# Performance work log

Hardware: AMD Instinct MI355X
Metric: run time of the kernel (lower is better)

## Reference

```python
import jax, jax.numpy as jnp
import numpy as np
import math

B, N, T, CI, CO = 4, 2048, 64, 32, 32
K, TAU = 6, 3


def _cheb(x, gso, k_order):
    # x: [b,n,t,c] complex, gso: [n,n] complex -> [K,b,n,t,c]
    polys = [x]
    if k_order > 1:
        polys.append(jnp.einsum('nm,bmtc->bntc', gso, x))
    for _ in range(2, k_order):
        polys.append(2.0 * jnp.einsum('nm,bmtc->bntc', gso, polys[-1]) - polys[-2])
    return jnp.stack(polys)


def _lag(p, tau):
    # shift along time axis (-2) by tau, zero-padding at the front
    if tau == 0:
        return p
    pad = jnp.zeros_like(p[..., :tau, :])
    return jnp.concatenate([pad, p[..., :-tau, :]], axis=-2)


def setup_inputs() -> dict:
    key = jax.random.key(0)
    ks = jax.random.split(key, 6)
    scale = 1.0 / math.sqrt(K * TAU * CI)
    gso_scale = 0.5 / math.sqrt(N)  # keep spectral radius ~<=1 for Cheb recursion
    return {
        'x_real': jax.random.normal(ks[0], (B, N, T, CI), jnp.float32),
        'x_imag': jax.random.normal(ks[1], (B, N, T, CI), jnp.float32),
        'gso_real': jax.random.normal(ks[2], (N, N), jnp.float32) * gso_scale,
        'gso_imag': jax.random.normal(ks[3], (N, N), jnp.float32) * gso_scale,
        'weight_real': jax.random.uniform(ks[4], (K, TAU, CI, CO), jnp.float32, -scale, scale),
        'weight_imag': jax.random.uniform(ks[5], (K, TAU, CI, CO), jnp.float32, -scale, scale),
        'bias_real': jnp.zeros((CO,), jnp.float32),
        'bias_imag': jnp.zeros((CO,), jnp.float32),
    }


def reference(x_real, x_imag, gso_real, gso_imag, weight_real, weight_imag, bias_real, bias_imag):
    x = jax.lax.complex(x_real, x_imag)
    gso = jax.lax.complex(gso_real, gso_imag)
    w = jax.lax.complex(weight_real, weight_imag)  # [K,TAU,i,o]
    bias = jax.lax.complex(bias_real, bias_imag)
    # Lag (time shift) and the graph shift act on different axes, so they
    # commute: compute the Chebyshev recursion ONCE on x, then lag the
    # stacked polynomials — same math as cheb(lag(x)) in the original.
    polys = _cheb(x, gso, K)  # [K,b,n,t,c]
    out = jnp.zeros((B, N, T, CO), dtype=polys.dtype)
    for tau in range(TAU):
        out = out + jnp.einsum('kbnti,kio->bnto', _lag(polys, tau), w[:, tau])
    return out + bias
```

## Files before the change

kernel.cpp:

```cpp
#include <hip/hip_runtime.h>
#include <stdint.h>

#define Bn 4
#define Nn 2048
#define Tn 64
#define CIn 32
#define COn 32
#define Kn 6
#define TAUn 3
#define Jn 8192

typedef _Float16 f16;
typedef _Float16 f16x2 __attribute__((ext_vector_type(2)));
typedef _Float16 f16x4 __attribute__((ext_vector_type(4)));
typedef _Float16 f16x8 __attribute__((ext_vector_type(8)));
typedef float f32x4 __attribute__((ext_vector_type(4)));

#if defined(__has_builtin)
#if __has_builtin(__builtin_amdgcn_fdot2)
#define HAVE_FDOT2 1
#endif
#endif

__device__ __forceinline__ float fdot2(f16x2 a, f16x2 b, float c) {
#ifdef HAVE_FDOT2
  return __builtin_amdgcn_fdot2(a, b, c, false);
#else
  return c + (float)a[0] * (float)b[0] + (float)a[1] * (float)b[1];
#endif
}

__device__ __forceinline__ void gld_lds16(const void* g, void* l) {
  auto gp = (const __attribute__((address_space(1))) uint32_t*)(uintptr_t)g;
  auto lp = (__attribute__((address_space(3))) uint32_t*)(uint32_t)(uintptr_t)l;
  __builtin_amdgcn_global_load_lds(gp, lp, 16, 0, 0);
}

__global__ __launch_bounds__(256) void pack_gso(const float* __restrict__ gr,
                                                const float* __restrict__ gi,
                                                f16* __restrict__ Gr,
                                                f16* __restrict__ Gi) {
  int u = blockIdx.x * 256 + threadIdx.x;
  float4 vr = ((const float4*)gr)[u];
  float4 vi = ((const float4*)gi)[u];
  f16x4 hr, hi;
  hr[0] = (f16)vr.x; hr[1] = (f16)vr.y; hr[2] = (f16)vr.z; hr[3] = (f16)vr.w;
  hi[0] = (f16)vi.x; hi[1] = (f16)vi.y; hi[2] = (f16)vi.z; hi[3] = (f16)vi.w;
  ((f16x4*)Gr)[u] = hr;
  ((f16x4*)Gi)[u] = hi;
}

__global__ __launch_bounds__(256) void pack_x(const float* __restrict__ xr,
                                              const float* __restrict__ xi,
                                              f16* __restrict__ P0) {
  __shared__ float tile[64][65];
  const int t = threadIdx.x;
  const int q0 = blockIdx.x * 64;
  const int n0 = blockIdx.y * 64;
  const int b = blockIdx.z;
  const int rr = t >> 4;
  const int cc = (t & 15) * 4;
  #pragma unroll
  for (int plane = 0; plane < 2; ++plane) {
    const float* src = plane ? xi : xr;
    if (plane) __syncthreads();
    #pragma unroll
    for (int it = 0; it < 4; ++it) {
      int n = it * 16 + rr;
      float4 v = *(const float4*)(src + ((size_t)b * Nn + n0 + n) * 2048 + q0 + cc);
      tile[n][cc + 0] = v.x; tile[n][cc + 1] = v.y;
      tile[n][cc + 2] = v.z; tile[n][cc + 3] = v.w;
    }
    __syncthreads();
    #pragma unroll
    for (int it = 0; it < 4; ++it) {
      int q = it * 16 + rr;
      f16x4 hv;
      hv[0] = (f16)tile[cc + 0][q];
      hv[1] = (f16)tile[cc + 1][q];
      hv[2] = (f16)tile[cc + 2][q];
      hv[3] = (f16)tile[cc + 3][q];
      *(f16x4*)(P0 + ((size_t)b * 2048 + q0 + q) * 4096 + plane * 2048 + n0 + cc) = hv;
    }
  }
}

__global__ __launch_bounds__(256) void pack_w(const float* __restrict__ wr,
                                              const float* __restrict__ wi,
                                              uint2* __restrict__ wpk) {
  int idx = blockIdx.x * 256 + threadIdx.x;
  if (idx >= Kn * TAUn * CIn * COn) return;
  float r = wr[idx], i = wi[idx];
  uint16_t hr = __builtin_bit_cast(uint16_t, (f16)r);
  uint16_t hi = __builtin_bit_cast(uint16_t, (f16)i);
  uint16_t hni = __builtin_bit_cast(uint16_t, (f16)(-i));
  uint2 o;
  o.x = (uint32_t)hr | ((uint32_t)hni << 16);
  o.y = (uint32_t)hi | ((uint32_t)hr << 16);
  wpk[idx] = o;
}

template <int MODE>
__global__ __launch_bounds__(512, 2) void cheb_gemm(
    const f16* __restrict__ Gr, const f16* __restrict__ Gi,
    const f16* __restrict__ P, f16* __restrict__ Q) {
  extern __shared__ __align__(16) char lds[];
  f16* L = (f16*)lds;

  const int tid = threadIdx.x;
  const int lane = tid & 63;
  const int w = tid >> 6;
  const int sub = lane >> 4, rr = lane & 15;

  const int bid = blockIdx.x;
  const int xcd = bid & 7;
  const int l = bid >> 3;
  const int bj = xcd * 4 + (l >> 4);
  const int bn = l & 15;
  const int n0 = bn * 256, j0 = bj * 256;
  const bool top = n0 < 2048;
  const int gmbase = n0 & 2047;

  auto stageA = [&](const f16* plane, int kcol, int h, int slot) {
    #pragma unroll
    for (int p = 0; p < 2; ++p) {
      int u = p * 512 + tid;
      int row = u & 127, ch = u >> 7;
      const f16* src = plane + (size_t)(gmbase + h * 128 + row) * 2048 + kcol + ch * 8;
      gld_lds16(src, L + slot * 8192 + (u - lane) * 8);
    }
  };
  auto stageB = [&](int kt, int h, int slot) {
    #pragma unroll
    for (int p = 0; p < 2; ++p) {
      int u = p * 512 + tid;
      int row = u & 127, ch = u >> 7;
      const f16* src = P + (size_t)(j0 + h * 128 + row) * 4096 + kt * 64 + ch * 8;
      gld_lds16(src, L + slot * 8192 + (u - lane) * 8);
    }
  };
  auto Aplane = [&](int kt) -> const f16* {
    bool kr = (kt & 32) != 0;
    return top ? (kr ? Gi : Gr) : (kr ? Gr : Gi);
  };

  f32x4 acc[16][2] = {};
  f16x8 bfr[2][2];

  stageB(0, 0, 4); stageB(0, 1, 5);
  stageA(Aplane(0), 0, 0, 0); stageA(Aplane(0), 0, 1, 1);

  for (int kt = 0; kt < 64; ++kt) {
    const int cur = kt & 1;
    const int nxt = cur ^ 1;
    const int ktn = (kt + 1) & 63;
    const f16* apn = Aplane(ktn);
    const int kcoln = (ktn * 64) & 2047;
    const bool negA = top && (kt & 32);

    asm volatile("s_waitcnt vmcnt(2)" ::: "memory");
    __builtin_amdgcn_s_barrier();

    #pragma unroll
    for (int p = 0; p < 4; ++p) {
      if (p == 2) {
        asm volatile("s_waitcnt vmcnt(4)" ::: "memory");
        __builtin_amdgcn_s_barrier();
      }
      f16x8 afr[4][2];
      const int slotA = cur * 2 + (p >> 1);
      #pragma unroll
      for (int f = 0; f < 4; ++f) {
        int fr = p * 4 + f;
        int r128 = (fr & 7) * 16 + rr;
        #pragma unroll
        for (int ks = 0; ks < 2; ++ks)
          afr[f][ks] = *(const f16x8*)(L + slotA * 8192 + ((ks * 4 + sub) * 128 + r128) * 8);
      }
      if (p == 0) {
        const int slotB = 4 + cur * 2 + (w >> 2);
        const int rB = (w & 3) * 32 + rr;
        #pragma unroll
        for (int fc = 0; fc < 2; ++fc)
          #pragma unroll
          for (int ks = 0; ks < 2; ++ks)
            bfr[fc][ks] = *(const f16x8*)(L + slotB * 8192 + ((ks * 4 + sub) * 128 + rB + fc * 16) * 8);
      }
      if (p == 0) stageB(ktn, 0, 4 + nxt * 2);
      if (p == 1) stageB(ktn, 1, 5 + nxt * 2);
      if (p == 2) stageA(apn, kcoln, 0, nxt * 2);
      if (p == 3) stageA(apn, kcoln, 1, nxt * 2 + 1);
      if (negA) {
        #pragma unroll
        for (int f = 0; f < 4; ++f) { afr[f][0] = -afr[f][0]; afr[f][1] = -afr[f][1]; }
      }
      __builtin_amdgcn_s_setprio(1);
      #pragma unroll
      for (int f = 0; f < 4; ++f)
        #pragma unroll
        for (int fc = 0; fc < 2; ++fc)
          #pragma unroll
          for (int ks = 0; ks < 2; ++ks)
            acc[p * 4 + f][fc] = __builtin_amdgcn_mfma_f32_16x16x32_f16(
                afr[f][ks], bfr[fc][ks], acc[p * 4 + f][fc], 0, 0, 0);
      __builtin_amdgcn_s_setprio(0);
    }
  }

  asm volatile("s_waitcnt vmcnt(0)" ::: "memory");

  #pragma unroll
  for (int fc = 0; fc < 2; ++fc) {
    size_t j = (size_t)j0 + w * 32 + fc * 16 + (lane & 15);
    #pragma unroll
    for (int fr = 0; fr < 16; ++fr) {
      int nn = n0 + fr * 16 + ((lane >> 4) << 2);
      size_t off = j * 4096 + nn;
      f16x4 v;
      if (MODE == 1) {
        f16x4 o = *(const f16x4*)(Q + off);
        #pragma unroll
        for (int r = 0; r < 4; ++r)
          v[r] = (f16)(2.0f * acc[fr][fc][r] - (float)o[r]);
      } else {
        #pragma unroll
        for (int r = 0; r < 4; ++r)
          v[r] = (f16)acc[fr][fc][r];
      }
      *(f16x4*)(Q + off) = v;
    }
  }
}

template <bool CPLX>
__global__ __launch_bounds__(256, 4) void contract_k(
    const f16* __restrict__ Pc, const uint2* __restrict__ wpk,
    const float* __restrict__ biasr, const float* __restrict__ biasi,
    float* __restrict__ out, int k) {
  __shared__ __align__(16) uint32_t Plds[96 * 64];
  __shared__ __align__(16) uint32_t WA[96 * 32];
  __shared__ __align__(16) uint32_t WB[CPLX ? 96 * 32 : 32];

  const int t = threadIdx.x;
  const int n0 = blockIdx.x * 64;
  const int tt = blockIdx.y;
  const int b = blockIdx.z;

  #pragma unroll
  for (int it = 0; it < 3; ++it) {
    int task = it * 256 + t;
    int row = task >> 3, oc = task & 7;
    int tp = (tt - 2) * 32 + row;
    uint4 ur = {0, 0, 0, 0}, ui = {0, 0, 0, 0};
    if (tp >= 0) {
      size_t goff = ((size_t)b * 2048 + tp) * 4096 + n0 + oc * 8;
      ur = *(const uint4*)(Pc + goff);
      ui = *(const uint4*)(Pc + goff + 2048);
    }
    uint32_t* dst = &Plds[row * 64 + oc * 8];
    dst[0] = (ur.x & 0xffffu) | (ui.x << 16);
    dst[1] = (ur.x >> 16) | (ui.x & 0xffff0000u);
    dst[2] = (ur.y & 0xffffu) | (ui.y << 16);
    dst[3] = (ur.y >> 16) | (ui.y & 0xffff0000u);
    dst[4] = (ur.z & 0xffffu) | (ui.z << 16);
    dst[5] = (ur.z >> 16) | (ui.z & 0xffff0000u);
    dst[6] = (ur.w & 0xffffu) | (ui.w << 16);
    dst[7] = (ur.w >> 16) | (ui.w & 0xffff0000u);
  }
  #pragma unroll
  for (int it = 0; it < 12; ++it) {
    int idx = it * 256 + t;
    int q = idx >> 5, o = idx & 31;
    int tau = 2 - (q >> 5), ci = q & 31;
    uint2 wv = wpk[((k * TAUn + tau) * CIn + ci) * COn + o];
    WA[idx] = wv.x;
    if (CPLX) WB[idx] = wv.y;
  }
  __syncthreads();

  const int no = t & 7, ng = t >> 3;
  float aR[8] = {0, 0, 0, 0, 0, 0, 0, 0};
  float aI[8] = {0, 0, 0, 0, 0, 0, 0, 0};
  for (int q = 0; q < 96; ++q) {
    uint2 pp = *(const uint2*)&Plds[q * 64 + ng * 2];
    f16x2 h0 = __builtin_bit_cast(f16x2, pp.x);
    f16x2 h1 = __builtin_bit_cast(f16x2, pp.y);
    uint4 wa = *(const uint4*)&WA[q * 32 + no * 4];
    const uint32_t* wap = &wa.x;
    #pragma unroll
    for (int c = 0; c < 4; ++c) {
      f16x2 wv = __builtin_bit_cast(f16x2, wap[c]);
      aR[c] = fdot2(h0, wv, aR[c]);
      aR[4 + c] = fdot2(h1, wv, aR[4 + c]);
    }
    if (CPLX) {
      uint4 wb = *(const uint4*)&WB[q * 32 + no * 4];
      const uint32_t* wbp = &wb.x;
      #pragma unroll
      for (int c = 0; c < 4; ++c) {
        f16x2 wv = __builtin_bit_cast(f16x2, wbp[c]);
        aI[c] = fdot2(h0, wv, aI[c]);
        aI[4 + c] = fdot2(h1, wv, aI[4 + c]);
      }
    }
  }

  #pragma unroll
  for (int a = 0; a < 2; ++a) {
    size_t n = (size_t)n0 + ng * 2 + a;
    size_t ob = (((size_t)b * Nn + n) * Tn + tt) * COn + no * 4;
    if (!CPLX) {
      float4 v;
      v.x = aR[a * 4 + 0]; v.y = aR[a * 4 + 1];
      v.z = aR[a * 4 + 2]; v.w = aR[a * 4 + 3];
      float4 cur;
      if (k == 0) cur = *(const float4*)(biasr + no * 4);
      else cur = *(const float4*)(out + ob);
      v.x += cur.x; v.y += cur.y; v.z += cur.z; v.w += cur.w;
      *(float4*)(out + ob) = v;
    } else {
      float* po = out + ob * 2;
      float4 lo, hi;
      lo.x = aR[a * 4 + 0]; lo.y = aI[a * 4 + 0];
      lo.z = aR[a * 4 + 1]; lo.w = aI[a * 4 + 1];
      hi.x = aR[a * 4 + 2]; hi.y = aI[a * 4 + 2];
      hi.z = aR[a * 4 + 3]; hi.w = aI[a * 4 + 3];
      float4 c0, c1;
      if (k == 0) {
        const float* pr = biasr + no * 4;
        const float* pi = biasi + no * 4;
        c0 = make_float4(pr[0], pi[0], pr[1], pi[1]);
        c1 = make_float4(pr[2], pi[2], pr[3], pi[3]);
      } else {
        c0 = *(const float4*)(po);
        c1 = *(const float4*)(po + 4);
      }
      lo.x += c0.x; lo.y += c0.y; lo.z += c0.z; lo.w += c0.w;
      hi.x += c1.x; hi.y += c1.y; hi.z += c1.z; hi.w += c1.w;
      *(float4*)(po) = lo;
      *(float4*)(po + 4) = hi;
    }
  }
}

extern "C" void kernel_launch(void* const* d_in, const int* in_sizes, int n_in,
                              void* d_out, int out_size, void* d_ws, size_t ws_size,
                              hipStream_t stream) {
  (void)in_sizes; (void)n_in;
  const float* xr = (const float*)d_in[0];
  const float* xi = (const float*)d_in[1];
  const float* gr = (const float*)d_in[2];
  const float* gi = (const float*)d_in[3];
  const float* wr = (const float*)d_in[4];
  const float* wi = (const float*)d_in[5];
  const float* biasr = (const float*)d_in[6];
  const float* biasi = (const float*)d_in[7];
  float* out = (float*)d_out;

  const size_t PPLANE = (size_t)Jn * 4096 * sizeof(f16);
  const size_t GPLANE = (size_t)Nn * Nn * sizeof(f16);
  const size_t WPK = (size_t)Kn * TAUn * CIn * COn * 8;
  if (ws_size < 2 * PPLANE + 2 * GPLANE + WPK) return;

  char* ws = (char*)d_ws;
  f16* P0 = (f16*)(ws);
  f16* P1 = (f16*)(ws + PPLANE);
  f16* Gr = (f16*)(ws + 2 * PPLANE);
  f16* Gi = (f16*)(ws + 2 * PPLANE + GPLANE);
  uint2* wpk = (uint2*)(ws + 2 * PPLANE + 2 * GPLANE);

  const bool cplx = (out_size == 2 * Bn * Nn * Tn * COn);

  pack_gso<<<dim3(4096), dim3(256), 0, stream>>>(gr, gi, Gr, Gi);
  pack_x<<<dim3(32, 32, 4), dim3(256), 0, stream>>>(xr, xi, P0);
  pack_w<<<dim3(72), dim3(256), 0, stream>>>(wr, wi, wpk);

  #define CONTRACT(KK, Pp)                                                         \
    do {                                                                           \
      if (cplx)                                                                    \
        contract_k<true><<<dim3(32, 64, 4), dim3(256), 0, stream>>>(               \
            Pp, wpk, biasr, biasi, out, KK);                                       \
      else                                                                         \
        contract_k<false><<<dim3(32, 64, 4), dim3(256), 0, stream>>>(              \
            Pp, wpk, biasr, biasi, out, KK);                                       \
    } while (0)

  CONTRACT(0, P0);
  cheb_gemm<0><<<dim3(512), dim3(512), 131072, stream>>>(Gr, Gi, P0, P1);
  CONTRACT(1, P1);
  cheb_gemm<1><<<dim3(512), dim3(512), 131072, stream>>>(Gr, Gi, P1, P0);
  CONTRACT(2, P0);
  cheb_gemm<1><<<dim3(512), dim3(512), 131072, stream>>>(Gr, Gi, P0, P1);
  CONTRACT(3, P1);
  cheb_gemm<1><<<dim3(512), dim3(512), 131072, stream>>>(Gr, Gi, P1, P0);
  CONTRACT(4, P0);
  cheb_gemm<1><<<dim3(512), dim3(512), 131072, stream>>>(Gr, Gi, P0, P1);
  CONTRACT(5, P1);
  #undef CONTRACT
}
```

Measured before the change: 2.179 ms.

## Retile cheb GEMM warps as 2x4 grid and split LDS stages along K

Changes the per-warp output tile from 256x32 to 128x64 (2x4 warp grid), which reduces the total A and B fragment loads from LDS per k-step. Staging now splits each 64-wide K tile into two 32-wide halves covering all 256 rows, instead of two 128-row halves, so each p-phase consumes one K half with a single MFMA k-step. This changes the global-load access pattern (shorter contiguous runs per row) and the barrier/wait dependencies between stages, so the pipelining and correctness of the wait counts must still hold.

```diff
diff --git a/kernel.cpp b/kernel.cpp
--- a/kernel.cpp
+++ b/kernel.cpp
@@ -110,6 +110,8 @@
   const int tid = threadIdx.x;
   const int lane = tid & 63;
   const int w = tid >> 6;
+  const int wm = w >> 2;
+  const int wn = w & 3;
   const int sub = lane >> 4, rr = lane & 15;
 
   const int bid = blockIdx.x;
@@ -125,8 +127,8 @@
     #pragma unroll
     for (int p = 0; p < 2; ++p) {
       int u = p * 512 + tid;
-      int row = u & 127, ch = u >> 7;
-      const f16* src = plane + (size_t)(gmbase + h * 128 + row) * 2048 + kcol + ch * 8;
+      int row = u & 255, c = u >> 8;
+      const f16* src = plane + (size_t)(gmbase + row) * 2048 + kcol + h * 32 + c * 8;
       gld_lds16(src, L + slot * 8192 + (u - lane) * 8);
     }
   };
@@ -134,8 +136,8 @@
     #pragma unroll
     for (int p = 0; p < 2; ++p) {
       int u = p * 512 + tid;
-      int row = u & 127, ch = u >> 7;
-      const f16* src = P + (size_t)(j0 + h * 128 + row) * 4096 + kt * 64 + ch * 8;
+      int row = u & 255, c = u >> 8;
+      const f16* src = P + (size_t)(j0 + row) * 4096 + kt * 64 + h * 32 + c * 8;
       gld_lds16(src, L + slot * 8192 + (u - lane) * 8);
     }
   };
@@ -144,8 +146,8 @@
     return top ? (kr ? Gi : Gr) : (kr ? Gr : Gi);
   };
 
-  f32x4 acc[16][2] = {};
-  f16x8 bfr[2][2];
+  f32x4 acc[8][4] = {};
+  f16x8 bfr[4];
 
   stageB(0, 0, 4); stageB(0, 1, 5);
   stageA(Aplane(0), 0, 0, 0); stageA(Aplane(0), 0, 1, 1);
@@ -157,6 +159,8 @@
     const f16* apn = Aplane(ktn);
     const int kcoln = (ktn * 64) & 2047;
     const bool negA = top && (kt & 32);
+    const int Abase = (cur * 2) * 8192;
+    const int Bbase = (4 + cur * 2) * 8192;
 
     asm volatile("s_waitcnt vmcnt(2)" ::: "memory");
     __builtin_amdgcn_s_barrier();
@@ -167,42 +171,37 @@
         asm volatile("s_waitcnt vmcnt(4)" ::: "memory");
         __builtin_amdgcn_s_barrier();
       }
-      f16x8 afr[4][2];
-      const int slotA = cur * 2 + (p >> 1);
+      const int ksh = p >> 1;
+      const int fh = p & 1;
+
+      if (fh == 0) {
+        #pragma unroll
+        for (int fc = 0; fc < 4; ++fc)
+          bfr[fc] = *(const f16x8*)(L + Bbase + ksh * 8192 +
+                                    (sub * 256 + wn * 64 + fc * 16 + rr) * 8);
+      }
+      f16x8 afr[4];
       #pragma unroll
-      for (int f = 0; f < 4; ++f) {
-        int fr = p * 4 + f;
-        int r128 = (fr & 7) * 16 + rr;
-        #pragma unroll
-        for (int ks = 0; ks < 2; ++ks)
-          afr[f][ks] = *(const f16x8*)(L + slotA * 8192 + ((ks * 4 + sub) * 128 + r128) * 8);
-      }
-      if (p == 0) {
-        const int slotB = 4 + cur * 2 + (w >> 2);
-        const int rB = (w & 3) * 32 + rr;
-        #pragma unroll
-        for (int fc = 0; fc < 2; ++fc)
-          #pragma unroll
-          for (int ks = 0; ks < 2; ++ks)
-            bfr[fc][ks] = *(const f16x8*)(L + slotB * 8192 + ((ks * 4 + sub) * 128 + rB + fc * 16) * 8);
-      }
+      for (int f = 0; f < 4; ++f)
+        afr[f] = *(const f16x8*)(L + Abase + ksh * 8192 +
+                                 (sub * 256 + wm * 128 + (fh * 4 + f) * 16 + rr) * 8);
+
       if (p == 0) stageB(ktn, 0, 4 + nxt * 2);
       if (p == 1) stageB(ktn, 1, 5 + nxt * 2);
       if (p == 2) stageA(apn, kcoln, 0, nxt * 2);
       if (p == 3) stageA(apn, kcoln, 1, nxt * 2 + 1);
+
       if (negA) {
         #pragma unroll
-        for (int f = 0; f < 4; ++f) { afr[f][0] = -afr[f][0]; afr[f][1] = -afr[f][1]; }
+        for (int f = 0; f < 4; ++f) afr[f] = -afr[f];
       }
       __builtin_amdgcn_s_setprio(1);
       #pragma unroll
       for (int f = 0; f < 4; ++f)
         #pragma unroll
-        for (int fc = 0; fc < 2; ++fc)
-          #pragma unroll
-          for (int ks = 0; ks < 2; ++ks)
-            acc[p * 4 + f][fc] = __builtin_amdgcn_mfma_f32_16x16x32_f16(
-                afr[f][ks], bfr[fc][ks], acc[p * 4 + f][fc], 0, 0, 0);
+        for (int fc = 0; fc < 4; ++fc)
+          acc[fh * 4 + f][fc] = __builtin_amdgcn_mfma_f32_16x16x32_f16(
+              afr[f], bfr[fc], acc[fh * 4 + f][fc], 0, 0, 0);
       __builtin_amdgcn_s_setprio(0);
     }
   }
@@ -210,11 +209,11 @@
   asm volatile("s_waitcnt vmcnt(0)" ::: "memory");
 
   #pragma unroll
-  for (int fc = 0; fc < 2; ++fc) {
-    size_t j = (size_t)j0 + w * 32 + fc * 16 + (lane & 15);
-    #pragma unroll
-    for (int fr = 0; fr < 16; ++fr) {
-      int nn = n0 + fr * 16 + ((lane >> 4) << 2);
+  for (int fc = 0; fc < 4; ++fc) {
+    size_t j = (size_t)j0 + wn * 64 + fc * 16 + (lane & 15);
+    #pragma unroll
+    for (int fr = 0; fr < 8; ++fr) {
+      int nn = n0 + wm * 128 + fr * 16 + ((lane >> 4) << 2);
       size_t off = j * 4096 + nn;
       f16x4 v;
       if (MODE == 1) {
```

Measured after the change: 2.280 ms. 1.05x slower.
